# Kernel tuning notes

Hardware: AMD Instinct MI355X
Metric: run time of the kernel (lower is better)

The kernel has to match this reference:

```python
import jax, jax.numpy as jnp
import numpy as np

EPS = 1e-6  # LayerNorm eps (norm_layer = partial(nn.LayerNorm, eps=1e-6))
B, CIN, HW, P, D, L, H, F = 32, 3, 224, 16, 768, 12, 12, 3072


def _ln(x, w, b):
    m = x.mean(-1, keepdims=True)
    v = jnp.var(x, axis=-1, keepdims=True)
    return (x - m) / jnp.sqrt(v + EPS) * w + b


def setup_inputs() -> dict:
    key = jax.random.key(0)
    ks = jax.random.split(key, 10)
    s = 0.02  # trunc_normal_ std
    N = (HW // P) ** 2
    return {
        "x": jax.random.normal(ks[0], (B, CIN, HW, HW), jnp.float32),
        "conv_w": jax.random.normal(ks[1], (D, CIN, P, P), jnp.float32) * s,
        "conv_b": jnp.zeros((D,), jnp.float32),
        "cls_token": jax.random.normal(ks[2], (1, 1, D), jnp.float32) * s,
        "pos_embed": jax.random.normal(ks[3], (1, N + 1, D), jnp.float32) * s,
        "ln1_w": jnp.ones((L, D), jnp.float32),
        "ln1_b": jnp.zeros((L, D), jnp.float32),
        "qkv_w": jax.random.normal(ks[4], (L, D, 3 * D), jnp.float32) * s,
        "qkv_b": jnp.zeros((L, 3 * D), jnp.float32),
        "proj_w": jax.random.normal(ks[5], (L, D, D), jnp.float32) * s,
        "proj_b": jnp.zeros((L, D), jnp.float32),
        "ln2_w": jnp.ones((L, D), jnp.float32),
        "ln2_b": jnp.zeros((L, D), jnp.float32),
        "fc1_w": jax.random.normal(ks[6], (L, D, F), jnp.float32) * s,
        "fc1_b": jnp.zeros((L, F), jnp.float32),
        "fc2_w": jax.random.normal(ks[7], (L, F, D), jnp.float32) * s,
        "fc2_b": jnp.zeros((L, D), jnp.float32),
        "lnf_w": jnp.ones((D,), jnp.float32),
        "lnf_b": jnp.zeros((D,), jnp.float32),
    }


def _vit(x, conv_w, conv_b, cls_token, pos_embed,
         ln1_w, ln1_b, qkv_w, qkv_b, proj_w, proj_b,
         ln2_w, ln2_b, fc1_w, fc1_b, fc2_w, fc2_b, lnf_w, lnf_b):
    b = x.shape[0]
    nh = HW // P
    dh = D // H
    scale = dh ** (-0.5)
    # Patch embed: stride-P/kernel-P conv == reshape into patches + GEMM.
    # [B,3,H,W] -> [B, nh*nh, 3*P*P] with (c,ph,pw) flatten order matching conv_w.
    p = x.reshape(b, CIN, nh, P, nh, P).transpose(0, 2, 4, 1, 3, 5)
    p = p.reshape(b, nh * nh, CIN * P * P)
    p = p @ conv_w.reshape(D, -1).T + conv_b  # [B, N, D]
    cls = jnp.broadcast_to(cls_token, (b, 1, D))
    h = jnp.concatenate([cls, p], axis=1) + pos_embed  # [B, N+1, D]

    def block(h, prm):
        l1w, l1b, qw, qb, pw, pb, l2w, l2b, f1w, f1b, f2w, f2b = prm
        y = _ln(h, l1w, l1b)
        qkv = (y @ qw + qb).reshape(b, -1, 3, H, dh)
        q, k, v = qkv[:, :, 0], qkv[:, :, 1], qkv[:, :, 2]  # [B,N,H,dh]
        attn = jnp.einsum("bnhd,bmhd->bhnm", q, k) * scale
        attn = jax.nn.softmax(attn, axis=-1)
        o = jnp.einsum("bhnm,bmhd->bnhd", attn, v).reshape(b, -1, D)
        h = h + (o @ pw + pb)
        y = _ln(h, l2w, l2b)
        h = h + (jax.nn.gelu(y @ f1w + f1b, approximate=False) @ f2w + f2b)
        return h, None

    prms = (ln1_w, ln1_b, qkv_w, qkv_b, proj_w, proj_b,
            ln2_w, ln2_b, fc1_w, fc1_b, fc2_w, fc2_b)
    h, _ = jax.lax.scan(block, h, prms)
    h = _ln(h, lnf_w, lnf_b)
    return h[:, 0][None]  # forward(): x.unsqueeze(0) -> [1, B, D]


def reference(x, conv_w, conv_b, cls_token, pos_embed,
              ln1_w, ln1_b, qkv_w, qkv_b, proj_w, proj_b,
              ln2_w, ln2_b, fc1_w, fc1_b, fc2_w, fc2_b, lnf_w, lnf_b):
    return _vit(x, conv_w, conv_b, cls_token, pos_embed,
                ln1_w, ln1_b, qkv_w, qkv_b, proj_w, proj_b,
                ln2_w, ln2_b, fc1_w, fc1_b, fc2_w, fc2_b, lnf_w, lnf_b)
```

## Files before the change

kernel.cpp:

```cpp
#include <hip/hip_runtime.h>
#include <cmath>

typedef __bf16 bf16;
typedef __bf16 bf16x8 __attribute__((ext_vector_type(8)));
typedef __bf16 bf16x4 __attribute__((ext_vector_type(4)));
typedef float  f32x4  __attribute__((ext_vector_type(4)));

#define MFMA16(a,b,c) __builtin_amdgcn_mfma_f32_16x16x32_bf16(a,b,c,0,0,0)

__device__ __forceinline__ void async_ld16(const void* g, void* l) {
  __builtin_amdgcn_global_load_lds((__attribute__((address_space(1))) void*)(g),
                                   (__attribute__((address_space(3))) void*)(l),
                                   16, 0, 0);
}

enum { EPI_PATCH = 0, EPI_BF16 = 1, EPI_RESID = 2, EPI_GELU = 3 };

template <int EPI, int TM>
__global__ __launch_bounds__(256) void gemm_bt(
    const bf16* __restrict__ A, const bf16* __restrict__ Wt,
    const float* __restrict__ bias, bf16* __restrict__ outB,
    float* __restrict__ outF, int M, int N, int K, int Kc)
{
  constexpr int MI = TM / 32;
  __shared__ bf16 As[TM * 32];
  __shared__ bf16 Bs[128 * 32];
  const int tid  = threadIdx.x;
  const int lane = tid & 63, wid = tid >> 6;
  const int qr   = lane & 15, quad = lane >> 4;
  const int wm   = wid >> 1, wn = wid & 1;
  const int bm   = blockIdx.x, bn = blockIdx.y, z = blockIdx.z;
  const int kbeg = z * Kc;
  const int kend = min(K, kbeg + Kc);
  const int sr   = wid * 16 + (lane >> 2);
  const int scol = (lane & 3) * 8;

  f32x4 zero4 = {0.f, 0.f, 0.f, 0.f};
  f32x4 acc[MI][4];
#pragma unroll
  for (int i = 0; i < MI; i++)
#pragma unroll
    for (int j = 0; j < 4; j++) acc[i][j] = zero4;

  int ra[TM / 64];
#pragma unroll
  for (int s = 0; s < TM / 64; s++)
    ra[s] = min(bm * TM + s * 64 + sr, M - 1);
  const size_t nr0 = (size_t)(bn * 128 + sr);
  const size_t nr1 = (size_t)(bn * 128 + 64 + sr);

  for (int k0 = kbeg; k0 < kend; k0 += 32) {
    __syncthreads();
#pragma unroll
    for (int s = 0; s < TM / 64; s++)
      async_ld16(A + (size_t)ra[s] * K + k0 + scol, &As[(s * 64 + wid * 16) * 32]);
    async_ld16(Wt + nr0 * K + k0 + scol, &Bs[(wid * 16) * 32]);
    async_ld16(Wt + nr1 * K + k0 + scol, &Bs[(64 + wid * 16) * 32]);
    __syncthreads();
    bf16x8 af[MI], bfr[4];
#pragma unroll
    for (int mi = 0; mi < MI; mi++)
      af[mi] = *(const bf16x8*)&As[(wm * (MI * 16) + mi * 16 + qr) * 32 + quad * 8];
#pragma unroll
    for (int ni = 0; ni < 4; ni++)
      bfr[ni] = *(const bf16x8*)&Bs[(wn * 64 + ni * 16 + qr) * 32 + quad * 8];
#pragma unroll
    for (int mi = 0; mi < MI; mi++)
#pragma unroll
      for (int ni = 0; ni < 4; ni++)
        acc[mi][ni] = MFMA16(af[mi], bfr[ni], acc[mi][ni]);
  }

#pragma unroll
  for (int mi = 0; mi < MI; mi++) {
#pragma unroll
    for (int ni = 0; ni < 4; ni++) {
      const int row0 = bm * TM + wm * (MI * 16) + mi * 16 + quad * 4;
      const int col  = bn * 128 + wn * 64 + ni * 16 + qr;
      const float bv = (z == 0) ? bias[col] : 0.f;
#pragma unroll
      for (int r = 0; r < 4; r++) {
        const int row = row0 + r;
        if (row < M) {
          float v = acc[mi][ni][r] + bv;
          if constexpr (EPI == EPI_PATCH) {
            int bb = row / 196, nn = row % 196;
            int orow = bb * 197 + 1 + nn;
            atomicAdd(&outF[(size_t)orow * 768 + col], v);
          } else if constexpr (EPI == EPI_BF16) {
            outB[(size_t)row * N + col] = (bf16)v;
          } else if constexpr (EPI == EPI_GELU) {
            float gel = 0.5f * v * (1.f + erff(v * 0.70710678118f));
            outB[(size_t)row * N + col] = (bf16)gel;
          } else {
            atomicAdd(&outF[(size_t)row * 768 + col], v);
          }
        }
      }
    }
  }
}

template <int EPI>
__global__ __launch_bounds__(512, 4) void gemm_bt8(
    const bf16* __restrict__ A, const bf16* __restrict__ Wt,
    const float* __restrict__ bias, bf16* __restrict__ outB,
    int M, int N, int K)
{
  __shared__ bf16 As[128 * 32];
  __shared__ bf16 Bs[128 * 32];
  const int tid  = threadIdx.x;
  const int lane = tid & 63, wid = tid >> 6;
  const int qr   = lane & 15, quad = lane >> 4;
  const int wm   = wid >> 1, wn = wid & 1;
  const int bm   = blockIdx.x, bn = blockIdx.y;
  const int sr   = wid * 16 + (lane >> 2);
  const int scol = (lane & 3) * 8;

  f32x4 zero4 = {0.f, 0.f, 0.f, 0.f};
  f32x4 acc[2][4];
#pragma unroll
  for (int i = 0; i < 2; i++)
#pragma unroll
    for (int j = 0; j < 4; j++) acc[i][j] = zero4;

  const int ra = min(bm * 128 + sr, M - 1);
  const size_t nr = (size_t)(bn * 128 + sr);

  for (int k0 = 0; k0 < K; k0 += 32) {
    __syncthreads();
    async_ld16(A  + (size_t)ra * K + k0 + scol, &As[(wid * 16) * 32]);
    async_ld16(Wt + nr * K + k0 + scol,         &Bs[(wid * 16) * 32]);
    __syncthreads();
    bf16x8 af[2], bfr[4];
#pragma unroll
    for (int mi = 0; mi < 2; mi++)
      af[mi] = *(const bf16x8*)&As[(wm * 32 + mi * 16 + qr) * 32 + quad * 8];
#pragma unroll
    for (int ni = 0; ni < 4; ni++)
      bfr[ni] = *(const bf16x8*)&Bs[(wn * 64 + ni * 16 + qr) * 32 + quad * 8];
#pragma unroll
    for (int mi = 0; mi < 2; mi++)
#pragma unroll
      for (int ni = 0; ni < 4; ni++)
        acc[mi][ni] = MFMA16(af[mi], bfr[ni], acc[mi][ni]);
  }

#pragma unroll
  for (int mi = 0; mi < 2; mi++) {
#pragma unroll
    for (int ni = 0; ni < 4; ni++) {
      const int row0 = bm * 128 + wm * 32 + mi * 16 + quad * 4;
      const int col  = bn * 128 + wn * 64 + ni * 16 + qr;
      const float bv = bias[col];
#pragma unroll
      for (int r = 0; r < 4; r++) {
        const int row = row0 + r;
        if (row < M) {
          float v = acc[mi][ni][r] + bv;
          if constexpr (EPI == EPI_GELU) {
            float gel = 0.5f * v * (1.f + erff(v * 0.70710678118f));
            outB[(size_t)row * N + col] = (bf16)gel;
          } else {
            outB[(size_t)row * N + col] = (bf16)v;
          }
        }
      }
    }
  }
}

__global__ __launch_bounds__(256) void attn_kernel(
    const bf16* __restrict__ qkv, bf16* __restrict__ o)
{
  __shared__ __align__(16) char smem[68864];
  bf16 (*Qs)[72]  = (bf16(*)[72])(smem);
  bf16 (*Ks)[72]  = (bf16(*)[72])(smem + 9216);
  bf16 (*Ps)[232] = (bf16(*)[232])(smem + 9216);
  bf16 (*Vt)[232] = (bf16(*)[232])(smem + 39168);

  const int tid  = threadIdx.x;
  const int lane = tid & 63, wid = tid >> 6;
  const int qr   = lane & 15, quad = lane >> 4;
  const int qt   = blockIdx.x & 3, bh = blockIdx.x >> 2;
  const int head = bh % 12, b = bh / 12;
  const int q0   = qt * 64;
  const size_t base = (size_t)b * 197 * 2304 + head * 64;

  {
    int r = tid >> 2, cb = (tid & 3) * 16;
    int s = q0 + r; if (s > 196) s = 196;
    const bf16* src = qkv + base + (size_t)s * 2304 + cb;
    *(uint4*)&Qs[r][cb]     = *(const uint4*)src;
    *(uint4*)&Qs[r][cb + 8] = *(const uint4*)(src + 8);
  }
  for (int rr = tid >> 2; rr < 208; rr += 64) {
    int cb = (tid & 3) * 16;
    uint4 v0 = make_uint4(0, 0, 0, 0), v1 = make_uint4(0, 0, 0, 0);
    if (rr < 197) {
      const bf16* src = qkv + base + 768 + (size_t)rr * 2304 + cb;
      v0 = *(const uint4*)src; v1 = *(const uint4*)(src + 8);
    }
    *(uint4*)&Ks[rr][cb] = v0; *(uint4*)&Ks[rr][cb + 8] = v1;
  }
  for (int rr = tid >> 2; rr < 224; rr += 64) {
    int cb = (tid & 3) * 16;
    bf16 tmp[16];
    if (rr < 197) {
      const bf16* src = qkv + base + 1536 + (size_t)rr * 2304 + cb;
      *(uint4*)&tmp[0] = *(const uint4*)src;
      *(uint4*)&tmp[8] = *(const uint4*)(src + 8);
    } else {
#pragma unroll
      for (int j = 0; j < 16; j++) tmp[j] = (bf16)0.f;
    }
#pragma unroll
    for (int j = 0; j < 16; j++) Vt[cb + j][rr] = tmp[j];
  }
  __syncthreads();

  bf16x8 qa0 = *(const bf16x8*)&Qs[wid * 16 + qr][quad * 8];
  bf16x8 qa1 = *(const bf16x8*)&Qs[wid * 16 + qr][32 + quad * 8];
  f32x4 zero4 = {0.f, 0.f, 0.f, 0.f};
  f32x4 sc[13];
#pragma unroll
  for (int t = 0; t < 13; t++) sc[t] = zero4;
#pragma unroll
  for (int t = 0; t < 13; t++) {
    bf16x8 kb0 = *(const bf16x8*)&Ks[t * 16 + qr][quad * 8];
    bf16x8 kb1 = *(const bf16x8*)&Ks[t * 16 + qr][32 + quad * 8];
    sc[t] = MFMA16(qa0, kb0, sc[t]);
    sc[t] = MFMA16(qa1, kb1, sc[t]);
  }
  float mx[4] = {-1e30f, -1e30f, -1e30f, -1e30f};
#pragma unroll
  for (int t = 0; t < 13; t++) {
    bool valid = (t * 16 + qr) < 197;
#pragma unroll
    for (int r = 0; r < 4; r++) {
      float v = sc[t][r] * 0.125f;
      sc[t][r] = v;
      if (valid) mx[r] = fmaxf(mx[r], v);
    }
  }
#pragma unroll
  for (int r = 0; r < 4; r++)
#pragma unroll
    for (int off = 1; off < 16; off <<= 1)
      mx[r] = fmaxf(mx[r], __shfl_xor(mx[r], off, 16));
  float sum[4] = {0.f, 0.f, 0.f, 0.f};
#pragma unroll
  for (int t = 0; t < 13; t++) {
    bool valid = (t * 16 + qr) < 197;
#pragma unroll
    for (int r = 0; r < 4; r++) {
      float e = valid ? __expf(sc[t][r] - mx[r]) : 0.f;
      sc[t][r] = e; sum[r] += e;
    }
  }
#pragma unroll
  for (int r = 0; r < 4; r++) {
#pragma unroll
    for (int off = 1; off < 16; off <<= 1)
      sum[r] += __shfl_xor(sum[r], off, 16);
    sum[r] = 1.f / sum[r];
  }
  __syncthreads();
#pragma unroll
  for (int t = 0; t < 13; t++)
#pragma unroll
    for (int r = 0; r < 4; r++)
      Ps[wid * 16 + quad * 4 + r][t * 16 + qr] = (bf16)(sc[t][r] * sum[r]);
  {
    bf16x4 zz = {(bf16)0.f, (bf16)0.f, (bf16)0.f, (bf16)0.f};
    *(bf16x4*)&Ps[wid * 16 + qr][208 + quad * 4] = zz;
  }
  __syncthreads();

  f32x4 oa[4];
#pragma unroll
  for (int ni = 0; ni < 4; ni++) oa[ni] = zero4;
#pragma unroll
  for (int k0 = 0; k0 < 224; k0 += 32) {
    bf16x8 pa = *(const bf16x8*)&Ps[wid * 16 + qr][k0 + quad * 8];
#pragma unroll
    for (int ni = 0; ni < 4; ni++) {
      bf16x8 vb = *(const bf16x8*)&Vt[ni * 16 + qr][k0 + quad * 8];
      oa[ni] = MFMA16(pa, vb, oa[ni]);
    }
  }
#pragma unroll
  for (int ni = 0; ni < 4; ni++)
#pragma unroll
    for (int r = 0; r < 4; r++) {
      int row = q0 + wid * 16 + quad * 4 + r;
      if (row < 197)
        o[(((size_t)b * 197 + row) * 12 + head) * 64 + ni * 16 + qr] =
            (bf16)oa[ni][r];
    }
}

__global__ __launch_bounds__(256) void ln_bf16(
    const float* __restrict__ h, const float* __restrict__ w,
    const float* __restrict__ b, bf16* __restrict__ y, int rows)
{
  int row = blockIdx.x * 4 + (threadIdx.x >> 6);
  int lane = threadIdx.x & 63;
  if (row >= rows) return;
  const float* hr = h + (size_t)row * 768;
  float v[12]; float s = 0.f;
#pragma unroll
  for (int i = 0; i < 12; i++) { v[i] = hr[lane + 64 * i]; s += v[i]; }
#pragma unroll
  for (int off = 32; off >= 1; off >>= 1) s += __shfl_xor(s, off, 64);
  float mean = s * (1.f / 768.f);
  float q = 0.f;
#pragma unroll
  for (int i = 0; i < 12; i++) { float d = v[i] - mean; q += d * d; }
#pragma unroll
  for (int off = 32; off >= 1; off >>= 1) q += __shfl_xor(q, off, 64);
  float rstd = rsqrtf(q * (1.f / 768.f) + 1e-6f);
  bf16* yr = y + (size_t)row * 768;
#pragma unroll
  for (int i = 0; i < 12; i++)
    yr[lane + 64 * i] = (bf16)((v[i] - mean) * rstd * w[lane + 64 * i] + b[lane + 64 * i]);
}

__global__ __launch_bounds__(256) void ln_final(
    const float* __restrict__ h, const float* __restrict__ w,
    const float* __restrict__ b, float* __restrict__ out)
{
  int bi = blockIdx.x * 4 + (threadIdx.x >> 6);
  int lane = threadIdx.x & 63;
  if (bi >= 32) return;
  const float* hr = h + (size_t)bi * 197 * 768;
  float v[12]; float s = 0.f;
#pragma unroll
  for (int i = 0; i < 12; i++) { v[i] = hr[lane + 64 * i]; s += v[i]; }
#pragma unroll
  for (int off = 32; off >= 1; off >>= 1) s += __shfl_xor(s, off, 64);
  float mean = s * (1.f / 768.f);
  float q = 0.f;
#pragma unroll
  for (int i = 0; i < 12; i++) { float d = v[i] - mean; q += d * d; }
#pragma unroll
  for (int off = 32; off >= 1; off >>= 1) q += __shfl_xor(q, off, 64);
  float rstd = rsqrtf(q * (1.f / 768.f) + 1e-6f);
#pragma unroll
  for (int i = 0; i < 12; i++)
    out[(size_t)bi * 768 + lane + 64 * i] =
        (v[i] - mean) * rstd * w[lane + 64 * i] + b[lane + 64 * i];
}

__global__ __launch_bounds__(256) void transpose_w(
    const float* __restrict__ in, bf16* __restrict__ out, int R, int C)
{
  __shared__ float t[32][33];
  size_t zoff = (size_t)blockIdx.z * R * C;
  in += zoff; out += zoff;
  int c0 = blockIdx.x * 32, r0 = blockIdx.y * 32;
  int lx = threadIdx.x & 31, ly = threadIdx.x >> 5;
#pragma unroll
  for (int i = 0; i < 32; i += 8) t[ly + i][lx] = in[(size_t)(r0 + ly + i) * C + c0 + lx];
  __syncthreads();
#pragma unroll
  for (int i = 0; i < 32; i += 8)
    out[(size_t)(c0 + ly + i) * R + r0 + lx] = (bf16)t[lx][ly + i];
}

__global__ __launch_bounds__(256) void convert_bf16(
    const float* __restrict__ in, bf16* __restrict__ out, int n)
{
  int i = blockIdx.x * 256 + threadIdx.x;
  if (i < n) out[i] = (bf16)in[i];
}

__global__ __launch_bounds__(256) void patch_extract(
    const float* __restrict__ x, bf16* __restrict__ patches)
{
  int i = blockIdx.x * 256 + threadIdx.x;
  if (i >= 6272 * 192) return;
  int m = i / 192, kq = (i % 192) * 4;
  int b = m / 196, pp = m % 196, py = pp / 14, px = pp % 14;
  int c = kq >> 8, rem = kq & 255, iy = rem >> 4, ix = rem & 15;
  const float4 v = *(const float4*)&x[(((size_t)(b * 3 + c) * 224 + py * 16 + iy) * 224) + px * 16 + ix];
  bf16x4 pv = {(bf16)v.x, (bf16)v.y, (bf16)v.z, (bf16)v.w};
  *(bf16x4*)&patches[(size_t)m * 768 + kq] = pv;
}

__global__ __launch_bounds__(256) void h_init_full(
    const float* __restrict__ cls, const float* __restrict__ pos,
    float* __restrict__ h)
{
  int i = blockIdx.x * 256 + threadIdx.x;
  if (i >= 6304 * 192) return;
  int row = i / 192, c4 = (i % 192) * 4;
  int s = row % 197;
  float4 pv = *(const float4*)&pos[(size_t)s * 768 + c4];
  if (s == 0) {
    float4 cv = *(const float4*)&cls[c4];
    pv.x += cv.x; pv.y += cv.y; pv.z += cv.z; pv.w += cv.w;
  }
  *(float4*)&h[(size_t)row * 768 + c4] = pv;
}

extern "C" void kernel_launch(void* const* d_in, const int* in_sizes, int n_in,
                              void* d_out, int out_size, void* d_ws, size_t ws_size,
                              hipStream_t stream)
{
  const float* x      = (const float*)d_in[0];
  const float* conv_w = (const float*)d_in[1];
  const float* conv_b = (const float*)d_in[2];
  const float* cls    = (const float*)d_in[3];
  const float* pos    = (const float*)d_in[4];
  const float* ln1_w  = (const float*)d_in[5];
  const float* ln1_b  = (const float*)d_in[6];
  const float* qkv_w  = (const float*)d_in[7];
  const float* qkv_b  = (const float*)d_in[8];
  const float* proj_w = (const float*)d_in[9];
  const float* proj_b = (const float*)d_in[10];
  const float* ln2_w  = (const float*)d_in[11];
  const float* ln2_b  = (const float*)d_in[12];
  const float* fc1_w  = (const float*)d_in[13];
  const float* fc1_b  = (const float*)d_in[14];
  const float* fc2_w  = (const float*)d_in[15];
  const float* fc2_b  = (const float*)d_in[16];
  const float* lnf_w  = (const float*)d_in[17];
  const float* lnf_b  = (const float*)d_in[18];
  float* out = (float*)d_out;
  (void)in_sizes; (void)n_in; (void)out_size; (void)ws_size;

  char* ws = (char*)d_ws;
  size_t off = 0;
  auto alloc = [&](size_t bytes) -> char* {
    char* p = ws + off;
    off += (bytes + 255) & ~(size_t)255;
    return p;
  };

  bf16*  convwB  = (bf16*)alloc((size_t)768 * 768 * 2);
  bf16*  qkvT    = (bf16*)alloc((size_t)12 * 2304 * 768 * 2);
  bf16*  projT   = (bf16*)alloc((size_t)12 * 768 * 768 * 2);
  bf16*  fc1T    = (bf16*)alloc((size_t)12 * 3072 * 768 * 2);
  bf16*  fc2T    = (bf16*)alloc((size_t)12 * 768 * 3072 * 2);
  bf16*  patches = (bf16*)alloc((size_t)6272 * 768 * 2);
  float* h       = (float*)alloc((size_t)6304 * 768 * 4);
  bf16*  y       = (bf16*)alloc((size_t)6304 * 768 * 2);
  bf16*  qkvB    = (bf16*)alloc((size_t)6304 * 2304 * 2);
  bf16*  obuf    = (bf16*)alloc((size_t)6304 * 768 * 2);
  bf16*  g       = (bf16*)alloc((size_t)6304 * 3072 * 2);

  convert_bf16<<<(768 * 768 + 255) / 256, 256, 0, stream>>>(conv_w, convwB, 768 * 768);
  transpose_w<<<dim3(2304 / 32, 768 / 32, 12), 256, 0, stream>>>(qkv_w, qkvT, 768, 2304);
  transpose_w<<<dim3(768 / 32, 768 / 32, 12), 256, 0, stream>>>(proj_w, projT, 768, 768);
  transpose_w<<<dim3(3072 / 32, 768 / 32, 12), 256, 0, stream>>>(fc1_w, fc1T, 768, 3072);
  transpose_w<<<dim3(768 / 32, 3072 / 32, 12), 256, 0, stream>>>(fc2_w, fc2T, 3072, 768);

  patch_extract<<<(6272 * 192) / 256, 256, 0, stream>>>(x, patches);
  h_init_full<<<(6304 * 192 + 255) / 256, 256, 0, stream>>>(cls, pos, h);
  gemm_bt<EPI_PATCH, 64><<<dim3(98, 6, 1), 256, 0, stream>>>(
      patches, convwB, conv_b, nullptr, h, 6272, 768, 768, 768);

  for (int l = 0; l < 12; l++) {
    ln_bf16<<<1576, 256, 0, stream>>>(h, ln1_w + l * 768, ln1_b + l * 768, y, 6304);
    gemm_bt8<EPI_BF16><<<dim3(50, 18), 512, 0, stream>>>(
        y, qkvT + (size_t)l * 2304 * 768, qkv_b + l * 2304, qkvB,
        6304, 2304, 768);
    attn_kernel<<<32 * 12 * 4, 256, 0, stream>>>(qkvB, obuf);
    gemm_bt<EPI_RESID, 64><<<dim3(99, 6, 1), 256, 0, stream>>>(
        obuf, projT + (size_t)l * 768 * 768, proj_b + l * 768, nullptr, h,
        6304, 768, 768, 768);
    ln_bf16<<<1576, 256, 0, stream>>>(h, ln2_w + l * 768, ln2_b + l * 768, y, 6304);
    gemm_bt8<EPI_GELU><<<dim3(50, 24), 512, 0, stream>>>(
        y, fc1T + (size_t)l * 3072 * 768, fc1_b + l * 3072, g,
        6304, 3072, 768);
    gemm_bt<EPI_RESID, 64><<<dim3(99, 6, 2), 256, 0, stream>>>(
        g, fc2T + (size_t)l * 768 * 3072, fc2_b + l * 768, nullptr, h,
        6304, 768, 3072, 1536);
  }
  ln_final<<<8, 256, 0, stream>>>(h, lnf_w, lnf_b, out);
}
```

Measured before the change: 3.706 ms.

## Double-buffer LDS tiles in GEMMs and enlarge residual GEMM tile to 128x128

Both GEMM kernels now keep two LDS buffers and issue the async global-to-LDS load for the next K-slice before computing on the current one, leaving one barrier per iteration instead of two. The residual and patch GEMMs switch from 64-row tiles to 128x128 tiles with a 4x4 MFMA accumulator per wave. Launch grids change to match, and the proj and patch GEMMs now use split-K of 2 with atomic accumulation. This aims to hide global load latency and raise MFMA reuse per loaded byte, at the cost of doubled LDS use, more registers and fewer blocks per launch.

```diff
diff --git a/kernel.cpp b/kernel.cpp
--- a/kernel.cpp
+++ b/kernel.cpp
@@ -16,15 +16,14 @@
 
 enum { EPI_PATCH = 0, EPI_BF16 = 1, EPI_RESID = 2, EPI_GELU = 3 };
 
-template <int EPI, int TM>
-__global__ __launch_bounds__(256) void gemm_bt(
+template <int EPI>
+__global__ __launch_bounds__(256) void gemm128(
     const bf16* __restrict__ A, const bf16* __restrict__ Wt,
     const float* __restrict__ bias, bf16* __restrict__ outB,
     float* __restrict__ outF, int M, int N, int K, int Kc)
 {
-  constexpr int MI = TM / 32;
-  __shared__ bf16 As[TM * 32];
-  __shared__ bf16 Bs[128 * 32];
+  __shared__ bf16 As[2][128 * 32];
+  __shared__ bf16 Bs[2][128 * 32];
   const int tid  = threadIdx.x;
   const int lane = tid & 63, wid = tid >> 6;
   const int qr   = lane & 15, quad = lane >> 4;
@@ -36,46 +35,51 @@
   const int scol = (lane & 3) * 8;
 
   f32x4 zero4 = {0.f, 0.f, 0.f, 0.f};
-  f32x4 acc[MI][4];
-#pragma unroll
-  for (int i = 0; i < MI; i++)
+  f32x4 acc[4][4];
+#pragma unroll
+  for (int i = 0; i < 4; i++)
 #pragma unroll
     for (int j = 0; j < 4; j++) acc[i][j] = zero4;
 
-  int ra[TM / 64];
-#pragma unroll
-  for (int s = 0; s < TM / 64; s++)
-    ra[s] = min(bm * TM + s * 64 + sr, M - 1);
+  const int ra0 = min(bm * 128 + sr, M - 1);
+  const int ra1 = min(bm * 128 + 64 + sr, M - 1);
   const size_t nr0 = (size_t)(bn * 128 + sr);
   const size_t nr1 = (size_t)(bn * 128 + 64 + sr);
 
+  auto stage = [&](int buf, int k0) {
+    async_ld16(A + (size_t)ra0 * K + k0 + scol, &As[buf][(wid * 16) * 32]);
+    async_ld16(A + (size_t)ra1 * K + k0 + scol, &As[buf][(64 + wid * 16) * 32]);
+    async_ld16(Wt + nr0 * K + k0 + scol, &Bs[buf][(wid * 16) * 32]);
+    async_ld16(Wt + nr1 * K + k0 + scol, &Bs[buf][(64 + wid * 16) * 32]);
+  };
+
+  stage(0, kbeg);
+  __syncthreads();
+  int cur = 0;
   for (int k0 = kbeg; k0 < kend; k0 += 32) {
-    __syncthreads();
-#pragma unroll
-    for (int s = 0; s < TM / 64; s++)
-      async_ld16(A + (size_t)ra[s] * K + k0 + scol, &As[(s * 64 + wid * 16) * 32]);
-    async_ld16(Wt + nr0 * K + k0 + scol, &Bs[(wid * 16) * 32]);
-    async_ld16(Wt + nr1 * K + k0 + scol, &Bs[(64 + wid * 16) * 32]);
-    __syncthreads();
-    bf16x8 af[MI], bfr[4];
-#pragma unroll
-    for (int mi = 0; mi < MI; mi++)
-      af[mi] = *(const bf16x8*)&As[(wm * (MI * 16) + mi * 16 + qr) * 32 + quad * 8];
+    const int kn = k0 + 32;
+    if (kn < kend) stage(cur ^ 1, kn);
+    bf16x8 af[4], bfr[4];
+#pragma unroll
+    for (int mi = 0; mi < 4; mi++)
+      af[mi] = *(const bf16x8*)&As[cur][(wm * 64 + mi * 16 + qr) * 32 + quad * 8];
 #pragma unroll
     for (int ni = 0; ni < 4; ni++)
-      bfr[ni] = *(const bf16x8*)&Bs[(wn * 64 + ni * 16 + qr) * 32 + quad * 8];
-#pragma unroll
-    for (int mi = 0; mi < MI; mi++)
+      bfr[ni] = *(const bf16x8*)&Bs[cur][(wn * 64 + ni * 16 + qr) * 32 + quad * 8];
+#pragma unroll
+    for (int mi = 0; mi < 4; mi++)
 #pragma unroll
       for (int ni = 0; ni < 4; ni++)
         acc[mi][ni] = MFMA16(af[mi], bfr[ni], acc[mi][ni]);
-  }
-
-#pragma unroll
-  for (int mi = 0; mi < MI; mi++) {
+    __syncthreads();
+    cur ^= 1;
+  }
+
+#pragma unroll
+  for (int mi = 0; mi < 4; mi++) {
 #pragma unroll
     for (int ni = 0; ni < 4; ni++) {
-      const int row0 = bm * TM + wm * (MI * 16) + mi * 16 + quad * 4;
+      const int row0 = bm * 128 + wm * 64 + mi * 16 + quad * 4;
       const int col  = bn * 128 + wn * 64 + ni * 16 + qr;
       const float bv = (z == 0) ? bias[col] : 0.f;
 #pragma unroll
@@ -107,8 +111,8 @@
     const float* __restrict__ bias, bf16* __restrict__ outB,
     int M, int N, int K)
 {
-  __shared__ bf16 As[128 * 32];
-  __shared__ bf16 Bs[128 * 32];
+  __shared__ bf16 As[2][128 * 32];
+  __shared__ bf16 Bs[2][128 * 32];
   const int tid  = threadIdx.x;
   const int lane = tid & 63, wid = tid >> 6;
   const int qr   = lane & 15, quad = lane >> 4;
@@ -127,23 +131,31 @@
   const int ra = min(bm * 128 + sr, M - 1);
   const size_t nr = (size_t)(bn * 128 + sr);
 
+  auto stage = [&](int buf, int k0) {
+    async_ld16(A  + (size_t)ra * K + k0 + scol, &As[buf][(wid * 16) * 32]);
+    async_ld16(Wt + nr * K + k0 + scol,         &Bs[buf][(wid * 16) * 32]);
+  };
+
+  stage(0, 0);
+  __syncthreads();
+  int cur = 0;
   for (int k0 = 0; k0 < K; k0 += 32) {
-    __syncthreads();
-    async_ld16(A  + (size_t)ra * K + k0 + scol, &As[(wid * 16) * 32]);
-    async_ld16(Wt + nr * K + k0 + scol,         &Bs[(wid * 16) * 32]);
-    __syncthreads();
+    const int kn = k0 + 32;
+    if (kn < K) stage(cur ^ 1, kn);
     bf16x8 af[2], bfr[4];
 #pragma unroll
     for (int mi = 0; mi < 2; mi++)
-      af[mi] = *(const bf16x8*)&As[(wm * 32 + mi * 16 + qr) * 32 + quad * 8];
+      af[mi] = *(const bf16x8*)&As[cur][(wm * 32 + mi * 16 + qr) * 32 + quad * 8];
 #pragma unroll
     for (int ni = 0; ni < 4; ni++)
-      bfr[ni] = *(const bf16x8*)&Bs[(wn * 64 + ni * 16 + qr) * 32 + quad * 8];
+      bfr[ni] = *(const bf16x8*)&Bs[cur][(wn * 64 + ni * 16 + qr) * 32 + quad * 8];
 #pragma unroll
     for (int mi = 0; mi < 2; mi++)
 #pragma unroll
       for (int ni = 0; ni < 4; ni++)
         acc[mi][ni] = MFMA16(af[mi], bfr[ni], acc[mi][ni]);
+    __syncthreads();
+    cur ^= 1;
   }
 
 #pragma unroll
@@ -458,8 +470,8 @@
 
   patch_extract<<<(6272 * 192) / 256, 256, 0, stream>>>(x, patches);
   h_init_full<<<(6304 * 192 + 255) / 256, 256, 0, stream>>>(cls, pos, h);
-  gemm_bt<EPI_PATCH, 64><<<dim3(98, 6, 1), 256, 0, stream>>>(
-      patches, convwB, conv_b, nullptr, h, 6272, 768, 768, 768);
+  gemm128<EPI_PATCH><<<dim3(49, 6, 2), 256, 0, stream>>>(
+      patches, convwB, conv_b, nullptr, h, 6272, 768, 768, 384);
 
   for (int l = 0; l < 12; l++) {
     ln_bf16<<<1576, 256, 0, stream>>>(h, ln1_w + l * 768, ln1_b + l * 768, y, 6304);
@@ -467,14 +479,14 @@
         y, qkvT + (size_t)l * 2304 * 768, qkv_b + l * 2304, qkvB,
         6304, 2304, 768);
     attn_kernel<<<32 * 12 * 4, 256, 0, stream>>>(qkvB, obuf);
-    gemm_bt<EPI_RESID, 64><<<dim3(99, 6, 1), 256, 0, stream>>>(
+    gemm128<EPI_RESID><<<dim3(50, 6, 2), 256, 0, stream>>>(
         obuf, projT + (size_t)l * 768 * 768, proj_b + l * 768, nullptr, h,
-        6304, 768, 768, 768);
+        6304, 768, 768, 384);
     ln_bf16<<<1576, 256, 0, stream>>>(h, ln2_w + l * 768, ln2_b + l * 768, y, 6304);
     gemm_bt8<EPI_GELU><<<dim3(50, 24), 512, 0, stream>>>(
         y, fc1T + (size_t)l * 3072 * 768, fc1_b + l * 3072, g,
         6304, 3072, 768);
-    gemm_bt<EPI_RESID, 64><<<dim3(99, 6, 2), 256, 0, stream>>>(
+    gemm128<EPI_RESID><<<dim3(50, 6, 2), 256, 0, stream>>>(
         g, fc2T + (size_t)l * 768 * 3072, fc2_b + l * 768, nullptr, h,
         6304, 768, 3072, 1536);
   }
```

After: 3.749 ms. About the same (+1.2%).
